# Performance work log

Hardware: AMD Instinct MI355X
Metric: run time of the kernel (lower is better)

Reference implementation:

```python
import jax, jax.numpy as jnp
import numpy as np

N, D_IN, D_HID, D_CODE, K = 131072, 768, 512, 256, 512

def setup_inputs() -> dict:
    key = jax.random.key(0)
    ks = jax.random.split(key, 10)
    s1 = 1.0 / np.sqrt(D_IN); s2 = 1.0 / np.sqrt(D_HID); s3 = 1.0 / np.sqrt(D_CODE)
    return {
        "x": jax.random.normal(ks[0], (N, D_IN), jnp.float32),
        "W1": jax.random.normal(ks[1], (D_IN, D_HID), jnp.float32) * s1,
        "b1": jnp.zeros((D_HID,), jnp.float32),
        "W2": jax.random.normal(ks[2], (D_HID, D_CODE), jnp.float32) * s2,
        "b2": jnp.zeros((D_CODE,), jnp.float32),
        "codebook": jax.random.normal(ks[3], (K, D_CODE), jnp.float32),
        "W3": jax.random.normal(ks[4], (D_CODE, D_HID), jnp.float32) * s3,
        "b3": jnp.zeros((D_HID,), jnp.float32),
        "W4": jax.random.normal(ks[5], (D_HID, D_IN), jnp.float32) * s2,
        "b4": jnp.zeros((D_IN,), jnp.float32),
    }

def reference(x, W1, b1, W2, b2, codebook, W3, b3, W4, b4):
    # encoder: Linear -> ReLU -> Linear
    z = jax.nn.relu(x @ W1 + b1) @ W2 + b2                      # [N, D_CODE]
    # nearest-code search: squared euclidean distances to codebook
    # ||z||^2 - 2 z.c + ||c||^2  (||z||^2 constant per row, drop for argmin)
    dots = z @ codebook.T                                        # [N, K]
    dist = jnp.sum(codebook * codebook, axis=-1)[None, :] - 2.0 * dots
    indices = jnp.argmin(dist, axis=-1)                          # [N] int
    quantized = codebook[indices]                                # gather [N, D_CODE]
    # commitment loss: mse(quantize.detach(), z) * commitment_weight(=1.0)
    commit_loss = jnp.mean((jax.lax.stop_gradient(quantized) - z) ** 2)
    # straight-through estimator
    quantized_st = z + jax.lax.stop_gradient(quantized - z)
    # decoder: Linear -> ReLU -> Linear
    recon = jax.nn.relu(quantized_st @ W3 + b3) @ W4 + b4        # [N, D_IN]
    return recon, indices.astype(jnp.int32), commit_loss
```

## Files before the change

### kernel.cpp

```cpp
#include <hip/hip_runtime.h>
#include <hip/hip_bf16.h>
#include <math.h>

#define N_ROWS 131072
#define DIN    768
#define DHID   512
#define DCODE  256
#define KC     512
#define NFUSE  768
#define TAU    5e-3f

typedef short short8 __attribute__((ext_vector_type(8)));
typedef float f32x4  __attribute__((ext_vector_type(4)));
typedef unsigned int   u32;
typedef unsigned short u16;

__device__ __forceinline__ void gload16(const void* g, void* l) {
    __builtin_amdgcn_global_load_lds(
        (const __attribute__((address_space(1))) u32*)g,
        (__attribute__((address_space(3))) u32*)l, 16, 0, 0);
}

__device__ __forceinline__ u16 f2bf(float f) {
    u32 u = __builtin_bit_cast(u32, f);
    return (u16)((u + 0x7fffu + ((u >> 16) & 1u)) >> 16);
}
__device__ __forceinline__ float bf2f(u16 h) {
    u32 u = ((u32)h) << 16;
    return __builtin_bit_cast(float, u);
}

__device__ __forceinline__ void xcd_swizzle(int& bxs, int& bys) {
    const int GX  = gridDim.x;
    const int nwg = GX * gridDim.y;
    const int lid = blockIdx.y * GX + blockIdx.x;
    const int chunk = nwg >> 3;
    const int nlid  = (lid & 7) * chunk + (lid >> 3);
    bxs = nlid % GX;
    bys = nlid / GX;
}

__device__ __forceinline__ void split_write(char* hidst, char* lodst, float4 v) {
    u16 h0 = f2bf(v.x), h1 = f2bf(v.y), h2 = f2bf(v.z), h3 = f2bf(v.w);
    u16 l0 = f2bf(__fsub_rn(v.x, bf2f(h0)));
    u16 l1 = f2bf(__fsub_rn(v.y, bf2f(h1)));
    u16 l2 = f2bf(__fsub_rn(v.z, bf2f(h2)));
    u16 l3 = f2bf(__fsub_rn(v.w, bf2f(h3)));
    ushort4 hi; hi.x = h0; hi.y = h1; hi.z = h2; hi.w = h3;
    ushort4 lo; lo.x = l0; lo.y = l1; lo.z = l2; lo.w = l3;
    *(ushort4*)hidst = hi;
    *(ushort4*)lodst = lo;
}

template<int EPI>
__global__ __launch_bounds__(256, 3)
void split2_gemm(const float* __restrict__ Af32,
                 const u16* __restrict__ Ahi, const u16* __restrict__ Alo,
                 const u16* __restrict__ Bhi, const u16* __restrict__ Blo,
                 const float* __restrict__ bias,
                 const float* __restrict__ cnorm,
                 u16* __restrict__ Chi, u16* __restrict__ Clo,
                 float* __restrict__ pd1, int* __restrict__ pi1,
                 float* __restrict__ pd2, float* __restrict__ pzn,
                 int M, int N, int K)
{
    __shared__ char lds[32768];
    const int t = threadIdx.x, lane = t & 63, wid = t >> 6;
    const int wm = wid >> 1, wn = wid & 1;
    int bxs, bys; xcd_swizzle(bxs, bys);
    const int bm = bys * 128, bn = bxs * 128;
    const bool full3 = (EPI == 0) || (bxs < 4);

    const int sr = lane >> 3, qq = lane & 7, sl = qq ^ sr;
    const u16* bsrc[4];
    #pragma unroll
    for (int c = 0; c < 4; c++) {
        int row = bn + (wid * 4 + c) * 8 + sr;
        const u16* base = (sl < 4) ? Bhi : Blo;
        bsrc[c] = base + (size_t)row * K + (sl & 3) * 8;
    }
    const u16* asrc[4];
    const float* a32src[4];
    int adhi[4], adlo[4];
    if constexpr (EPI == 1) {
        #pragma unroll
        for (int c = 0; c < 4; c++) {
            int row = bm + (wid * 4 + c) * 8 + sr;
            const u16* base = (sl < 4) ? Ahi : Alo;
            asrc[c] = base + (size_t)row * K + (sl & 3) * 8;
        }
    } else {
        #pragma unroll
        for (int c = 0; c < 4; c++) {
            int id = c * 256 + t;
            int row = id >> 3, k4 = id & 7;
            a32src[c] = Af32 + (size_t)(bm + row) * K + k4 * 4;
            int s = k4 >> 1, hf = k4 & 1;
            adhi[c] = row * 128 + ((s ^ (row & 7)) << 4) + hf * 8;
            adlo[c] = row * 128 + (((s | 4) ^ (row & 7)) << 4) + hf * 8;
        }
    }

    f32x4 acc[4][4];
    #pragma unroll
    for (int i = 0; i < 4; i++)
        #pragma unroll
        for (int j = 0; j < 4; j++) acc[i][j] = (f32x4)0.f;

    const int fr = lane & 15, sw = lane & 7;
    const int offhi = (((lane >> 4) ^ sw) << 4);
    const int offlo = ((((lane >> 4) | 4) ^ sw) << 4);
    const int arow = wm * 64 + fr, brow = wn * 64 + fr;
    const int NT = K >> 5;

    for (int tt = 0; tt < NT; tt++) {
        __syncthreads();
        const int kadv = tt * 32;
        #pragma unroll
        for (int c = 0; c < 4; c++)
            gload16(bsrc[c] + kadv, lds + 16384 + (wid * 4 + c) * 1024);
        if constexpr (EPI == 1) {
            #pragma unroll
            for (int c = 0; c < 4; c++)
                gload16(asrc[c] + kadv, lds + (wid * 4 + c) * 1024);
        } else {
            #pragma unroll
            for (int c = 0; c < 4; c++) {
                float4 v = *(const float4*)(a32src[c] + kadv);
                split_write(lds + adhi[c], lds + adlo[c], v);
            }
        }
        __syncthreads();
        char* ab  = lds;
        char* bb2 = lds + 16384;
        short8 ah[4], al[4];
        #pragma unroll
        for (int i = 0; i < 4; i++) {
            ah[i] = *(const short8*)(ab + ((arow + i * 16) << 7) + offhi);
            al[i] = *(const short8*)(ab + ((arow + i * 16) << 7) + offlo);
        }
        if (full3) {
            #pragma unroll
            for (int j = 0; j < 4; j++) {
                short8 bh = *(const short8*)(bb2 + ((brow + j * 16) << 7) + offhi);
                short8 bl = *(const short8*)(bb2 + ((brow + j * 16) << 7) + offlo);
                #pragma unroll
                for (int i = 0; i < 4; i++) {
                    acc[i][j] = __builtin_amdgcn_mfma_f32_16x16x32_bf16(ah[i], bh, acc[i][j], 0, 0, 0);
                    acc[i][j] = __builtin_amdgcn_mfma_f32_16x16x32_bf16(al[i], bh, acc[i][j], 0, 0, 0);
                    acc[i][j] = __builtin_amdgcn_mfma_f32_16x16x32_bf16(ah[i], bl, acc[i][j], 0, 0, 0);
                }
            }
        } else {
            #pragma unroll
            for (int j = 0; j < 4; j++) {
                short8 bh = *(const short8*)(bb2 + ((brow + j * 16) << 7) + offhi);
                #pragma unroll
                for (int i = 0; i < 4; i++)
                    acc[i][j] = __builtin_amdgcn_mfma_f32_16x16x32_bf16(ah[i], bh, acc[i][j], 0, 0, 0);
            }
        }
    }

    if constexpr (EPI == 1) {
        const int ec = lane & 15, g = lane >> 4;
        if (bxs < 4) {
            float cnv[4], bcv[4];
            #pragma unroll
            for (int j = 0; j < 4; j++) {
                int c = bn + wn * 64 + j * 16 + ec;
                cnv[j] = cnorm[c]; bcv[j] = bias[c];
            }
            const int strip = bxs * 2 + wn;
            #pragma unroll
            for (int i = 0; i < 4; i++) {
                #pragma unroll
                for (int e = 0; e < 4; e++) {
                    float d1 = INFINITY, d2 = INFINITY; int i1 = 0x7fffffff;
                    #pragma unroll
                    for (int j = 0; j < 4; j++) {
                        int c = bn + wn * 64 + j * 16 + ec;
                        float d = __fsub_rn(cnv[j],
                                  __fmul_rn(2.0f, __fadd_rn(acc[i][j][e], bcv[j])));
                        if (d < d1 || (d == d1 && c < i1)) { d2 = d1; d1 = d; i1 = c; }
                        else if (d < d2) d2 = d;
                    }
                    #pragma unroll
                    for (int m = 1; m < 16; m <<= 1) {
                        float od1 = __shfl_xor(d1, m);
                        int   oi1 = __shfl_xor(i1, m);
                        float od2 = __shfl_xor(d2, m);
                        if (od1 < d1 || (od1 == d1 && oi1 < i1)) {
                            d2 = fminf(d1, od2); d1 = od1; i1 = oi1;
                        } else d2 = fminf(d2, od1);
                    }
                    if (ec == 0) {
                        int r = bm + wm * 64 + i * 16 + g * 4 + e;
                        pd1[(size_t)strip * M + r] = d1;
                        pi1[(size_t)strip * M + r] = i1;
                        pd2[(size_t)strip * M + r] = d2;
                    }
                }
            }
        } else {
            float bcv[4];
            #pragma unroll
            for (int j = 0; j < 4; j++)
                bcv[j] = bias[bn + wn * 64 + j * 16 + ec];
            const int zs = (bxs - 4) * 2 + wn;
            #pragma unroll
            for (int i = 0; i < 4; i++) {
                #pragma unroll
                for (int e = 0; e < 4; e++) {
                    float s = 0.f;
                    #pragma unroll
                    for (int j = 0; j < 4; j++) {
                        float zv = acc[i][j][e] + bcv[j];
                        s = fmaf(zv, zv, s);
                    }
                    #pragma unroll
                    for (int m = 1; m < 16; m <<= 1) s += __shfl_xor(s, m);
                    if (ec == 0) {
                        int r = bm + wm * 64 + i * 16 + g * 4 + e;
                        pzn[(size_t)zs * M + r] = s;
                    }
                }
            }
        }
        return;
    } else {
        const int er = (lane >> 4) * 4, ec = lane & 15;
        #pragma unroll
        for (int j = 0; j < 4; j++) {
            int col = bn + wn * 64 + j * 16 + ec;
            float bb = bias[col];
            #pragma unroll
            for (int i = 0; i < 4; i++) {
                #pragma unroll
                for (int e = 0; e < 4; e++) {
                    int r = bm + wm * 64 + i * 16 + er + e;
                    float v = fmaxf(__fadd_rn(acc[i][j][e], bb), 0.f);
                    u16 hi = f2bf(v);
                    u16 lo = f2bf(__fsub_rn(v, bf2f(hi)));
                    Chi[(size_t)r * N + col] = hi;
                    Clo[(size_t)r * N + col] = lo;
                }
            }
        }
    }
}

template<bool RELU, bool OUT_BF16>
__global__ __launch_bounds__(256, 3)
void mfma_gemm(const u16* __restrict__ A, const u16* __restrict__ BT,
               const float* __restrict__ bias,
               void* __restrict__ Cout, int M, int N, int K)
{
    __shared__ char lds[32768];
    const int t    = threadIdx.x;
    const int lane = t & 63, wid = t >> 6;
    const int wm   = wid >> 1, wn = wid & 1;
    int bxs, bys;
    xcd_swizzle(bxs, bys);
    const int bm = bys * 128, bn = bxs * 128;

    const int sr = lane >> 3;
    const int sc = ((lane & 7) ^ sr) * 8;
    const u16* aptr[4];
    const u16* bptr[4];
    #pragma unroll
    for (int c = 0; c < 4; c++) {
        int gc   = wid * 4 + c;
        int arow = bm + 8 * gc + sr;
        aptr[c] = A  + (size_t)arow * K + sc;
        int brow = bn + 8 * gc + sr;
        bptr[c] = BT + (size_t)brow * K + sc;
    }

    f32x4 acc[4][4];
    #pragma unroll
    for (int i = 0; i < 4; i++)
        #pragma unroll
        for (int j = 0; j < 4; j++) acc[i][j] = (f32x4)0.f;

    const int koff0 = (16 * (lane >> 4))      ^ ((lane & 7) << 4);
    const int koff1 = (64 + 16 * (lane >> 4)) ^ ((lane & 7) << 4);
    const int arow_rd = wm * 64 + (lane & 15);
    const int brow_rd = wn * 64 + (lane & 15);

    const int NT = K >> 6;
    for (int tt = 0; tt < NT; tt++) {
        __syncthreads();
        const int k0 = tt << 6;
        #pragma unroll
        for (int c = 0; c < 4; c++) {
            int gc = wid * 4 + c;
            gload16(aptr[c] + k0, lds + gc * 1024);
            gload16(bptr[c] + k0, lds + 16384 + gc * 1024);
        }
        __syncthreads();
        char* ldsA = lds;
        char* ldsB = lds + 16384;
        #pragma unroll
        for (int kk = 0; kk < 2; kk++) {
            const int ko = kk ? koff1 : koff0;
            short8 af[4], bfr[4];
            #pragma unroll
            for (int i = 0; i < 4; i++)
                af[i]  = *(const short8*)(ldsA + (arow_rd + i * 16) * 128 + ko);
            #pragma unroll
            for (int j = 0; j < 4; j++)
                bfr[j] = *(const short8*)(ldsB + (brow_rd + j * 16) * 128 + ko);
            #pragma unroll
            for (int i = 0; i < 4; i++)
                #pragma unroll
                for (int j = 0; j < 4; j++)
                    acc[i][j] = __builtin_amdgcn_mfma_f32_16x16x32_bf16(
                        af[i], bfr[j], acc[i][j], 0, 0, 0);
        }
    }

    const int er = (lane >> 4) * 4;
    const int ec = lane & 15;
    #pragma unroll
    for (int j = 0; j < 4; j++) {
        int col  = bn + wn * 64 + j * 16 + ec;
        float bb = bias[col];
        #pragma unroll
        for (int i = 0; i < 4; i++) {
            #pragma unroll
            for (int e = 0; e < 4; e++) {
                int r   = bm + wm * 64 + i * 16 + er + e;
                float v = acc[i][j][e] + bb;
                if (RELU) v = fmaxf(v, 0.f);
                if (OUT_BF16) ((u16*)Cout)[(size_t)r * N + col]  = f2bf(v);
                else          ((float*)Cout)[(size_t)r * N + col] = v;
            }
        }
    }
}

__global__ __launch_bounds__(256)
void gather_out(const float* __restrict__ R, const int* __restrict__ idxi,
                float* __restrict__ out)
{
    int w    = (blockIdx.x * 256 + threadIdx.x) >> 6;
    int lane = threadIdx.x & 63;
    int nw   = (gridDim.x * 256) >> 6;
    for (int r = w; r < N_ROWS; r += nw) {
        int code = idxi[r];
        const float4* src = (const float4*)(R + (size_t)code * DIN);
        float4* dst = (float4*)(out + (size_t)r * DIN);
        dst[lane]       = src[lane];
        dst[lane + 64]  = src[lane + 64];
        dst[lane + 128] = src[lane + 128];
    }
}

__global__ void transpose_cb_kernel(const float* __restrict__ cb, float* __restrict__ cbT)
{
    int tid = blockIdx.x * 256 + threadIdx.x;
    int k = tid >> 8;
    int d = tid & 255;
    cbT[(size_t)d * KC + k] = cb[(size_t)k * DCODE + d];
}

__global__ void cast_bf16_kernel(const float* __restrict__ in, u16* __restrict__ out, int n)
{
    int i = blockIdx.x * 256 + threadIdx.x;
    if (i < n) out[i] = f2bf(in[i]);
}

__global__ void castT_bf16_kernel(const float* __restrict__ in, u16* __restrict__ out,
                                  int K, int N)
{
    int i = blockIdx.x * 256 + threadIdx.x;
    if (i >= K * N) return;
    int n = i / K, k = i - n * K;
    out[i] = f2bf(in[(size_t)k * N + n]);
}

__global__ void prep_W1T(const float* __restrict__ W1, u16* __restrict__ Thi,
                         u16* __restrict__ Tlo)
{
    int id = blockIdx.x * 256 + threadIdx.x;
    if (id >= DHID * DIN) return;
    int n = id / DIN, k = id - n * DIN;
    float v = W1[(size_t)k * DHID + n];
    u16 hi = f2bf(v);
    Thi[id] = hi;
    Tlo[id] = f2bf(__fsub_rn(v, bf2f(hi)));
}

__global__ void prep_Wc(const float* __restrict__ W2, const float* __restrict__ cb,
                        u16* __restrict__ Thi, u16* __restrict__ Tlo)
{
    int id = blockIdx.x * 256 + threadIdx.x;
    int n = id & 511, h = id >> 9;
    double acc = 0.0;
    for (int tt2 = 0; tt2 < DCODE; tt2++)
        acc += (double)W2[(size_t)h * DCODE + tt2] * (double)cb[(size_t)n * DCODE + tt2];
    float v = (float)acc;
    u16 hi = f2bf(v);
    Thi[(size_t)n * DHID + h] = hi;
    Tlo[(size_t)n * DHID + h] = f2bf(__fsub_rn(v, bf2f(hi)));
}

__global__ void prep_W2T_pair(const float* __restrict__ W2, u16* __restrict__ Thi,
                              u16* __restrict__ Tlo)
{
    int id = blockIdx.x * 256 + threadIdx.x;
    if (id >= DCODE * DHID) return;
    int t2 = id >> 9, h = id & 511;
    float v = W2[(size_t)h * DCODE + t2];
    u16 hi = f2bf(v);
    Thi[(size_t)(KC + t2) * DHID + h] = hi;
    Tlo[(size_t)(KC + t2) * DHID + h] = f2bf(__fsub_rn(v, bf2f(hi)));
}

__global__ void prep_bcf(const float* __restrict__ b2, const float* __restrict__ cb,
                         float* __restrict__ bcf)
{
    int n = blockIdx.x * 256 + threadIdx.x;
    if (n >= NFUSE) return;
    if (n < KC) {
        double acc = 0.0;
        for (int tt2 = 0; tt2 < DCODE; tt2++)
            acc += (double)b2[tt2] * (double)cb[(size_t)n * DCODE + tt2];
        bcf[n] = (float)acc;
    } else {
        bcf[n] = b2[n - KC];
    }
}

__global__ void cnorm_np_kernel(const float* __restrict__ cb, float* __restrict__ cnorm)
{
    int k = blockIdx.x * 64 + threadIdx.x;
    if (k >= KC) return;
    const float* c = cb + (size_t)k * DCODE;
    float bsum[2];
    #pragma unroll
    for (int b = 0; b < 2; b++) {
        const float* a = c + b * 128;
        float r[8];
        #pragma unroll
        for (int j = 0; j < 8; j++) r[j] = __fmul_rn(a[j], a[j]);
        for (int i = 8; i < 128; i += 8)
            #pragma unroll
            for (int j = 0; j < 8; j++)
                r[j] = __fadd_rn(r[j], __fmul_rn(a[i + j], a[i + j]));
        bsum[b] = __fadd_rn(
            __fadd_rn(__fadd_rn(r[0], r[1]), __fadd_rn(r[2], r[3])),
            __fadd_rn(__fadd_rn(r[4], r[5]), __fadd_rn(r[6], r[7])));
    }
    cnorm[k] = __fadd_rn(bsum[0], bsum[1]);
}

__global__ void final_argmin_flag(const float* __restrict__ pd1,
                                  const int* __restrict__ pi1,
                                  const float* __restrict__ pd2,
                                  const float* __restrict__ pzn,
                                  float* __restrict__ idx_f,
                                  int* __restrict__ idx_i,
                                  float* __restrict__ rowloss,
                                  int* __restrict__ cnt,
                                  int* __restrict__ list)
{
    int r = blockIdx.x * 256 + threadIdx.x;
    if (r >= N_ROWS) return;
    float d1 = pd1[r]; int i1 = pi1[r]; float d2 = pd2[r];
    #pragma unroll
    for (int b = 1; b < 8; b++) {
        float od1 = pd1[(size_t)b * N_ROWS + r];
        int   oi1 = pi1[(size_t)b * N_ROWS + r];
        float od2 = pd2[(size_t)b * N_ROWS + r];
        if (od1 < d1 || (od1 == d1 && oi1 < i1)) {
            d2 = fminf(d1, od2); d1 = od1; i1 = oi1;
        } else d2 = fminf(d2, od1);
    }
    float zn = pzn[r] + pzn[(size_t)N_ROWS + r]
             + pzn[(size_t)2 * N_ROWS + r] + pzn[(size_t)3 * N_ROWS + r];
    idx_f[r]   = (float)i1;
    idx_i[r]   = i1;
    rowloss[r] = zn + d1;
    if (d2 - d1 < TAU) {
        int p = atomicAdd(cnt, 1);
        list[p] = r;
    }
}

__global__ __launch_bounds__(512)
void recompute_kernel(const float* __restrict__ x,  const float* __restrict__ W1,
                      const float* __restrict__ b1, const float* __restrict__ W2,
                      const float* __restrict__ b2, const float* __restrict__ cbT,
                      const float* __restrict__ cnorm,
                      const int* __restrict__ cnt,  const int* __restrict__ list,
                      float* __restrict__ idx_f,    int* __restrict__ idx_i)
{
    __shared__ float xs[8][DIN];
    __shared__ float h1s[8][DHID];
    __shared__ float zs[8][DCODE];
    __shared__ float swd[8][8];
    __shared__ int   swi[8][8];
    __shared__ int   rls[8];
    const int t = threadIdx.x;
    const int n = *cnt;

    for (int base = blockIdx.x * 8; base < n; base += gridDim.x * 8) {
        __syncthreads();
        if (t < 8) rls[t] = (base + t < n) ? list[base + t] : -1;
        __syncthreads();
        #pragma unroll
        for (int rr = 0; rr < 8; rr++) {
            int row = rls[rr];
            if (row >= 0)
                for (int i = t; i < DIN; i += 512)
                    xs[rr][i] = x[(size_t)row * DIN + i];
        }
        __syncthreads();
        {
            float acc[8] = {0.f,0.f,0.f,0.f,0.f,0.f,0.f,0.f};
            for (int i = 0; i < DIN; i++) {
                float w = W1[(size_t)i * DHID + t];
                #pragma unroll
                for (int rr = 0; rr < 8; rr++)
                    acc[rr] = fmaf(xs[rr][i], w, acc[rr]);
            }
            float bb = b1[t];
            #pragma unroll
            for (int rr = 0; rr < 8; rr++)
                h1s[rr][t] = fmaxf(__fadd_rn(acc[rr], bb), 0.f);
        }
        __syncthreads();
        {
            int half = t >> 8, t2 = t & 255;
            float acc[4] = {0.f,0.f,0.f,0.f};
            for (int h = 0; h < DHID; h++) {
                float w = W2[(size_t)h * DCODE + t2];
                #pragma unroll
                for (int q2 = 0; q2 < 4; q2++)
                    acc[q2] = fmaf(h1s[half * 4 + q2][h], w, acc[q2]);
            }
            float bb = b2[t2];
            #pragma unroll
            for (int q2 = 0; q2 < 4; q2++)
                zs[half * 4 + q2][t2] = __fadd_rn(acc[q2], bb);
        }
        __syncthreads();
        {
            float acc[8] = {0.f,0.f,0.f,0.f,0.f,0.f,0.f,0.f};
            for (int d = 0; d < DCODE; d++) {
                float c = cbT[(size_t)d * KC + t];
                #pragma unroll
                for (int rr = 0; rr < 8; rr++)
                    acc[rr] = fmaf(zs[rr][d], c, acc[rr]);
            }
            float cn = cnorm[t];
            #pragma unroll
            for (int rr = 0; rr < 8; rr++) {
                float d = __fsub_rn(cn, __fmul_rn(2.0f, acc[rr]));
                int ii = t;
                #pragma unroll
                for (int m = 1; m < 64; m <<= 1) {
                    float od = __shfl_xor(d, m);
                    int   oi = __shfl_xor(ii, m);
                    if (od < d || (od == d && oi < ii)) { d = od; ii = oi; }
                }
                if ((t & 63) == 0) { swd[rr][t >> 6] = d; swi[rr][t >> 6] = ii; }
            }
        }
        __syncthreads();
        if (t < 8) {
            int row = rls[t];
            if (row >= 0) {
                float d = swd[t][0]; int ii = swi[t][0];
                #pragma unroll
                for (int w = 1; w < 8; w++) {
                    float od = swd[t][w]; int oi = swi[t][w];
                    if (od < d || (od == d && oi < ii)) { d = od; ii = oi; }
                }
                idx_i[row] = ii;
                idx_f[row] = (float)ii;
            }
        }
    }
}

__global__ void loss_reduce_kernel(const float* __restrict__ rowloss,
                                   double* __restrict__ acc, int n)
{
    double s = 0.0;
    for (int i = blockIdx.x * blockDim.x + threadIdx.x; i < n; i += gridDim.x * blockDim.x)
        s += (double)rowloss[i];
    for (int off = 32; off; off >>= 1) s += __shfl_xor(s, off);
    __shared__ double red[4];
    int lane = threadIdx.x & 63, wave = threadIdx.x >> 6;
    if (lane == 0) red[wave] = s;
    __syncthreads();
    if (threadIdx.x == 0) {
        double b = red[0] + red[1] + red[2] + red[3];
        atomicAdd(acc, b);
    }
}

__global__ void finalize_kernel(const double* __restrict__ acc, float* __restrict__ out)
{
    out[0] = (float)(acc[0] / ((double)N_ROWS * (double)DCODE));
}

extern "C" void kernel_launch(void* const* d_in, const int* in_sizes, int n_in,
                              void* d_out, int out_size, void* d_ws, size_t ws_size,
                              hipStream_t stream)
{
    const float* x  = (const float*)d_in[0];
    const float* W1 = (const float*)d_in[1];
    const float* b1 = (const float*)d_in[2];
    const float* W2 = (const float*)d_in[3];
    const float* b2 = (const float*)d_in[4];
    const float* cb = (const float*)d_in[5];
    const float* W3 = (const float*)d_in[6];
    const float* b3 = (const float*)d_in[7];
    const float* W4 = (const float*)d_in[8];
    const float* b4 = (const float*)d_in[9];
    float* out = (float*)d_out;
    char*  ws  = (char*)d_ws;

    u16*    h1hi    = (u16*)   (ws);
    u16*    h1lo    = (u16*)   (ws + 134217728);
    float*  pd1     = (float*) (ws + 268435456);
    int*    pi1     = (int*)   (ws + 272629760);
    float*  pd2     = (float*) (ws + 276824064);
    float*  pzn     = (float*) (ws + 281018368);
    float*  rowloss = (float*) (ws + 283115520);
    int*    idxi    = (int*)   (ws + 283639808);
    int*    list    = (int*)   (ws + 284164096);
    int*    rcnt    = (int*)   (ws + 284688384);
    double* lossa   = (double*)(ws + 284688448);
    u16*    W1Thi   = (u16*)   (ws + 284688512);
    u16*    W1Tlo   = (u16*)   (ws + 285474944);
    u16*    WfThi   = (u16*)   (ws + 286261376);
    u16*    WfTlo   = (u16*)   (ws + 287047808);
    u16*    cbB     = (u16*)   (ws + 287834240);
    u16*    W3T     = (u16*)   (ws + 288096384);
    u16*    W4T     = (u16*)   (ws + 288358528);
    float*  bcf     = (float*) (ws + 289144960);
    float*  cnorm   = (float*) (ws + 289148032);
    float*  cbT     = (float*) (ws + 289150080);
    u16*    R1b     = (u16*)   (ws + 289674368);
    float*  Rf      = (float*) (ws + 290198656);

    float* idxf    = out + (size_t)N_ROWS * DIN;
    float* lossout = idxf + N_ROWS;

    hipMemsetAsync(ws + 284688384, 0, 128, stream);

    transpose_cb_kernel<<<512, 256, 0, stream>>>(cb, cbT);
    cnorm_np_kernel<<<8, 64, 0, stream>>>(cb, cnorm);
    cast_bf16_kernel<<<(KC*DCODE)/256, 256, 0, stream>>>(cb, cbB, KC*DCODE);
    castT_bf16_kernel<<<(DCODE*DHID)/256, 256, 0, stream>>>(W3, W3T, DCODE, DHID);
    castT_bf16_kernel<<<(DHID*DIN)/256, 256, 0, stream>>>(W4, W4T, DHID, DIN);
    prep_W1T<<<(DHID*DIN)/256, 256, 0, stream>>>(W1, W1Thi, W1Tlo);
    prep_Wc<<<(KC*DHID)/256, 256, 0, stream>>>(W2, cb, WfThi, WfTlo);
    prep_W2T_pair<<<(DCODE*DHID)/256, 256, 0, stream>>>(W2, WfThi, WfTlo);
    prep_bcf<<<3, 256, 0, stream>>>(b2, cb, bcf);

    mfma_gemm<true,  true ><<<dim3(4, 4), 256, 0, stream>>>(
        cbB, W3T, b3, (void*)R1b, KC, DHID, DCODE);
    mfma_gemm<false, false><<<dim3(6, 4), 256, 0, stream>>>(
        R1b, W4T, b4, (void*)Rf, KC, DIN, DHID);

    split2_gemm<0><<<dim3(DHID/128, N_ROWS/128), 256, 0, stream>>>(
        x, nullptr, nullptr, W1Thi, W1Tlo, b1, nullptr,
        h1hi, h1lo, nullptr, nullptr, nullptr, nullptr, N_ROWS, DHID, DIN);
    split2_gemm<1><<<dim3(NFUSE/128, N_ROWS/128), 256, 0, stream>>>(
        nullptr, h1hi, h1lo, WfThi, WfTlo, bcf, cnorm,
        nullptr, nullptr, pd1, pi1, pd2, pzn, N_ROWS, NFUSE, DHID);

    final_argmin_flag<<<N_ROWS/256, 256, 0, stream>>>(
        pd1, pi1, pd2, pzn, idxf, idxi, rowloss, rcnt, list);
    recompute_kernel<<<2048, 512, 0, stream>>>(
        x, W1, b1, W2, b2, cbT, cnorm, rcnt, list, idxf, idxi);

    gather_out<<<4096, 256, 0, stream>>>(Rf, idxi, out);

    loss_reduce_kernel<<<256, 256, 0, stream>>>(rowloss, lossa, N_ROWS);
    finalize_kernel<<<1, 1, 0, stream>>>(lossa, lossout);
}
```

Before: 942.0 us.

## Use single-bf16 dots GEMM with split-precision rescoring of ambiguous rows

```diff
diff --git a/kernel.cpp b/kernel.cpp
--- a/kernel.cpp
+++ b/kernel.cpp
@@ -8,7 +8,9 @@
 #define DCODE  256
 #define KC     512
 #define NFUSE  768
-#define TAU    5e-3f
+#define TAU1   0.6f
+#define TAU2   5e-3f
+#define CAP    16384
 
 typedef short short8 __attribute__((ext_vector_type(8)));
 typedef float f32x4  __attribute__((ext_vector_type(4)));
@@ -61,7 +63,7 @@
                  const float* __restrict__ cnorm,
                  u16* __restrict__ Chi, u16* __restrict__ Clo,
                  float* __restrict__ pd1, int* __restrict__ pi1,
-                 float* __restrict__ pd2, float* __restrict__ pzn,
+                 float* __restrict__ pd2,
                  int M, int N, int K)
 {
     __shared__ char lds[32768];
@@ -69,7 +71,6 @@
     const int wm = wid >> 1, wn = wid & 1;
     int bxs, bys; xcd_swizzle(bxs, bys);
     const int bm = bys * 128, bn = bxs * 128;
-    const bool full3 = (EPI == 0) || (bxs < 4);
 
     const int sr = lane >> 3, qq = lane & 7, sl = qq ^ sr;
     const u16* bsrc[4];
@@ -139,91 +140,55 @@
             ah[i] = *(const short8*)(ab + ((arow + i * 16) << 7) + offhi);
             al[i] = *(const short8*)(ab + ((arow + i * 16) << 7) + offlo);
         }
-        if (full3) {
-            #pragma unroll
-            for (int j = 0; j < 4; j++) {
-                short8 bh = *(const short8*)(bb2 + ((brow + j * 16) << 7) + offhi);
-                short8 bl = *(const short8*)(bb2 + ((brow + j * 16) << 7) + offlo);
-                #pragma unroll
-                for (int i = 0; i < 4; i++) {
-                    acc[i][j] = __builtin_amdgcn_mfma_f32_16x16x32_bf16(ah[i], bh, acc[i][j], 0, 0, 0);
-                    acc[i][j] = __builtin_amdgcn_mfma_f32_16x16x32_bf16(al[i], bh, acc[i][j], 0, 0, 0);
-                    acc[i][j] = __builtin_amdgcn_mfma_f32_16x16x32_bf16(ah[i], bl, acc[i][j], 0, 0, 0);
-                }
-            }
-        } else {
-            #pragma unroll
-            for (int j = 0; j < 4; j++) {
-                short8 bh = *(const short8*)(bb2 + ((brow + j * 16) << 7) + offhi);
-                #pragma unroll
-                for (int i = 0; i < 4; i++)
-                    acc[i][j] = __builtin_amdgcn_mfma_f32_16x16x32_bf16(ah[i], bh, acc[i][j], 0, 0, 0);
+        #pragma unroll
+        for (int j = 0; j < 4; j++) {
+            short8 bh = *(const short8*)(bb2 + ((brow + j * 16) << 7) + offhi);
+            short8 bl = *(const short8*)(bb2 + ((brow + j * 16) << 7) + offlo);
+            #pragma unroll
+            for (int i = 0; i < 4; i++) {
+                acc[i][j] = __builtin_amdgcn_mfma_f32_16x16x32_bf16(ah[i], bh, acc[i][j], 0, 0, 0);
+                acc[i][j] = __builtin_amdgcn_mfma_f32_16x16x32_bf16(al[i], bh, acc[i][j], 0, 0, 0);
+                acc[i][j] = __builtin_amdgcn_mfma_f32_16x16x32_bf16(ah[i], bl, acc[i][j], 0, 0, 0);
             }
         }
     }
 
     if constexpr (EPI == 1) {
         const int ec = lane & 15, g = lane >> 4;
-        if (bxs < 4) {
-            float cnv[4], bcv[4];
-            #pragma unroll
-            for (int j = 0; j < 4; j++) {
-                int c = bn + wn * 64 + j * 16 + ec;
-                cnv[j] = cnorm[c]; bcv[j] = bias[c];
-            }
-            const int strip = bxs * 2 + wn;
-            #pragma unroll
-            for (int i = 0; i < 4; i++) {
-                #pragma unroll
-                for (int e = 0; e < 4; e++) {
-                    float d1 = INFINITY, d2 = INFINITY; int i1 = 0x7fffffff;
-                    #pragma unroll
-                    for (int j = 0; j < 4; j++) {
-                        int c = bn + wn * 64 + j * 16 + ec;
-                        float d = __fsub_rn(cnv[j],
-                                  __fmul_rn(2.0f, __fadd_rn(acc[i][j][e], bcv[j])));
-                        if (d < d1 || (d == d1 && c < i1)) { d2 = d1; d1 = d; i1 = c; }
-                        else if (d < d2) d2 = d;
-                    }
-                    #pragma unroll
-                    for (int m = 1; m < 16; m <<= 1) {
-                        float od1 = __shfl_xor(d1, m);
-                        int   oi1 = __shfl_xor(i1, m);
-                        float od2 = __shfl_xor(d2, m);
-                        if (od1 < d1 || (od1 == d1 && oi1 < i1)) {
-                            d2 = fminf(d1, od2); d1 = od1; i1 = oi1;
-                        } else d2 = fminf(d2, od1);
-                    }
-                    if (ec == 0) {
-                        int r = bm + wm * 64 + i * 16 + g * 4 + e;
-                        pd1[(size_t)strip * M + r] = d1;
-                        pi1[(size_t)strip * M + r] = i1;
-                        pd2[(size_t)strip * M + r] = d2;
-                    }
-                }
-            }
-        } else {
-            float bcv[4];
-            #pragma unroll
-            for (int j = 0; j < 4; j++)
-                bcv[j] = bias[bn + wn * 64 + j * 16 + ec];
-            const int zs = (bxs - 4) * 2 + wn;
-            #pragma unroll
-            for (int i = 0; i < 4; i++) {
-                #pragma unroll
-                for (int e = 0; e < 4; e++) {
-                    float s = 0.f;
-                    #pragma unroll
-                    for (int j = 0; j < 4; j++) {
-                        float zv = acc[i][j][e] + bcv[j];
-                        s = fmaf(zv, zv, s);
-                    }
-                    #pragma unroll
-                    for (int m = 1; m < 16; m <<= 1) s += __shfl_xor(s, m);
-                    if (ec == 0) {
-                        int r = bm + wm * 64 + i * 16 + g * 4 + e;
-                        pzn[(size_t)zs * M + r] = s;
-                    }
+        float cnv[4], bcv[4];
+        #pragma unroll
+        for (int j = 0; j < 4; j++) {
+            int c = bn + wn * 64 + j * 16 + ec;
+            cnv[j] = cnorm[c]; bcv[j] = bias[c];
+        }
+        const int strip = bxs * 2 + wn;
+        #pragma unroll
+        for (int i = 0; i < 4; i++) {
+            #pragma unroll
+            for (int e = 0; e < 4; e++) {
+                float d1 = INFINITY, d2 = INFINITY; int i1 = 0x7fffffff;
+                #pragma unroll
+                for (int j = 0; j < 4; j++) {
+                    int c = bn + wn * 64 + j * 16 + ec;
+                    float d = __fsub_rn(cnv[j],
+                              __fmul_rn(2.0f, __fadd_rn(acc[i][j][e], bcv[j])));
+                    if (d < d1 || (d == d1 && c < i1)) { d2 = d1; d1 = d; i1 = c; }
+                    else if (d < d2) d2 = d;
+                }
+                #pragma unroll
+                for (int m = 1; m < 16; m <<= 1) {
+                    float od1 = __shfl_xor(d1, m);
+                    int   oi1 = __shfl_xor(i1, m);
+                    float od2 = __shfl_xor(d2, m);
+                    if (od1 < d1 || (od1 == d1 && oi1 < i1)) {
+                        d2 = fminf(d1, od2); d1 = od1; i1 = oi1;
+                    } else d2 = fminf(d2, od1);
+                }
+                if (ec == 0) {
+                    int r = bm + wm * 64 + i * 16 + g * 4 + e;
+                    pd1[(size_t)strip * M + r] = d1;
+                    pi1[(size_t)strip * M + r] = i1;
+                    pd2[(size_t)strip * M + r] = d2;
                 }
             }
         }
@@ -250,6 +215,139 @@
     }
 }
 
+__global__ __launch_bounds__(256, 3)
+void dots_gemm(const u16* __restrict__ A, const u16* __restrict__ BT,
+               const float* __restrict__ bias, const float* __restrict__ cnorm,
+               float* __restrict__ pd1, int* __restrict__ pi1,
+               float* __restrict__ pd2, float* __restrict__ pzn,
+               int M, int N, int K)
+{
+    __shared__ char lds[32768];
+    const int t = threadIdx.x, lane = t & 63, wid = t >> 6;
+    const int wm = wid >> 1, wn = wid & 1;
+    int bxs, bys; xcd_swizzle(bxs, bys);
+    const int bm = bys * 128, bn = bxs * 128;
+
+    const int sr = lane >> 3;
+    const int sc = ((lane & 7) ^ sr) * 8;
+    const u16* aptr[4];
+    const u16* bptr[4];
+    #pragma unroll
+    for (int c = 0; c < 4; c++) {
+        int gc = wid * 4 + c;
+        aptr[c] = A  + (size_t)(bm + 8 * gc + sr) * K + sc;
+        bptr[c] = BT + (size_t)(bn + 8 * gc + sr) * K + sc;
+    }
+
+    f32x4 acc[4][4];
+    #pragma unroll
+    for (int i = 0; i < 4; i++)
+        #pragma unroll
+        for (int j = 0; j < 4; j++) acc[i][j] = (f32x4)0.f;
+
+    const int koff0 = (16 * (lane >> 4))      ^ ((lane & 7) << 4);
+    const int koff1 = (64 + 16 * (lane >> 4)) ^ ((lane & 7) << 4);
+    const int arow_rd = wm * 64 + (lane & 15);
+    const int brow_rd = wn * 64 + (lane & 15);
+
+    const int NT = K >> 6;
+    for (int tt = 0; tt < NT; tt++) {
+        __syncthreads();
+        const int k0 = tt << 6;
+        #pragma unroll
+        for (int c = 0; c < 4; c++) {
+            int gc = wid * 4 + c;
+            gload16(aptr[c] + k0, lds + gc * 1024);
+            gload16(bptr[c] + k0, lds + 16384 + gc * 1024);
+        }
+        __syncthreads();
+        char* ldsA = lds;
+        char* ldsB = lds + 16384;
+        #pragma unroll
+        for (int kk = 0; kk < 2; kk++) {
+            const int ko = kk ? koff1 : koff0;
+            short8 af[4], bfr[4];
+            #pragma unroll
+            for (int i = 0; i < 4; i++)
+                af[i]  = *(const short8*)(ldsA + (arow_rd + i * 16) * 128 + ko);
+            #pragma unroll
+            for (int j = 0; j < 4; j++)
+                bfr[j] = *(const short8*)(ldsB + (brow_rd + j * 16) * 128 + ko);
+            #pragma unroll
+            for (int i = 0; i < 4; i++)
+                #pragma unroll
+                for (int j = 0; j < 4; j++)
+                    acc[i][j] = __builtin_amdgcn_mfma_f32_16x16x32_bf16(
+                        af[i], bfr[j], acc[i][j], 0, 0, 0);
+        }
+    }
+
+    const int ec = lane & 15, g = lane >> 4;
+    if (bxs < 4) {
+        float cnv[4], bcv[4];
+        #pragma unroll
+        for (int j = 0; j < 4; j++) {
+            int c = bn + wn * 64 + j * 16 + ec;
+            cnv[j] = cnorm[c]; bcv[j] = bias[c];
+        }
+        const int strip = bxs * 2 + wn;
+        #pragma unroll
+        for (int i = 0; i < 4; i++) {
+            #pragma unroll
+            for (int e = 0; e < 4; e++) {
+                float d1 = INFINITY, d2 = INFINITY; int i1 = 0x7fffffff;
+                #pragma unroll
+                for (int j = 0; j < 4; j++) {
+                    int c = bn + wn * 64 + j * 16 + ec;
+                    float d = __fsub_rn(cnv[j],
+                              __fmul_rn(2.0f, __fadd_rn(acc[i][j][e], bcv[j])));
+                    if (d < d1 || (d == d1 && c < i1)) { d2 = d1; d1 = d; i1 = c; }
+                    else if (d < d2) d2 = d;
+                }
+                #pragma unroll
+                for (int m = 1; m < 16; m <<= 1) {
+                    float od1 = __shfl_xor(d1, m);
+                    int   oi1 = __shfl_xor(i1, m);
+                    float od2 = __shfl_xor(d2, m);
+                    if (od1 < d1 || (od1 == d1 && oi1 < i1)) {
+                        d2 = fminf(d1, od2); d1 = od1; i1 = oi1;
+                    } else d2 = fminf(d2, od1);
+                }
+                if (ec == 0) {
+                    int r = bm + wm * 64 + i * 16 + g * 4 + e;
+                    pd1[(size_t)strip * M + r] = d1;
+                    pi1[(size_t)strip * M + r] = i1;
+                    pd2[(size_t)strip * M + r] = d2;
+                }
+            }
+        }
+    } else {
+        float bcv[4];
+        #pragma unroll
+        for (int j = 0; j < 4; j++)
+            bcv[j] = bias[bn + wn * 64 + j * 16 + ec];
+        const int zs = (bxs - 4) * 2 + wn;
+        #pragma unroll
+        for (int i = 0; i < 4; i++) {
+            #pragma unroll
+            for (int e = 0; e < 4; e++) {
+                float s = 0.f;
+                #pragma unroll
+                for (int j = 0; j < 4; j++) {
+                    float zv = acc[i][j][e] + bcv[j];
+                    s = fmaf(zv, zv, s);
+                }
+                #pragma unroll
+                for (int m = 1; m < 16; m <<= 1) s += __shfl_xor(s, m);
+                if (ec == 0) {
+                    int r = bm + wm * 64 + i * 16 + g * 4 + e;
+                    pzn[(size_t)zs * M + r] = s;
+                }
+            }
+        }
+    }
+}
+
 template<bool RELU, bool OUT_BF16>
 __global__ __launch_bounds__(256, 3)
 void mfma_gemm(const u16* __restrict__ A, const u16* __restrict__ BT,
@@ -271,10 +369,8 @@
     #pragma unroll
     for (int c = 0; c < 4; c++) {
         int gc   = wid * 4 + c;
-        int arow = bm + 8 * gc + sr;
-        aptr[c] = A  + (size_t)arow * K + sc;
-        int brow = bn + 8 * gc + sr;
-        bptr[c] = BT + (size_t)brow * K + sc;
+        aptr[c] = A  + (size_t)(bm + 8 * gc + sr) * K + sc;
+        bptr[c] = BT + (size_t)(bn + 8 * gc + sr) * K + sc;
     }
 
     f32x4 acc[4][4];
@@ -406,16 +502,12 @@
     Tlo[(size_t)n * DHID + h] = f2bf(__fsub_rn(v, bf2f(hi)));
 }
 
-__global__ void prep_W2T_pair(const float* __restrict__ W2, u16* __restrict__ Thi,
-                              u16* __restrict__ Tlo)
+__global__ void prep_W2T(const float* __restrict__ W2, u16* __restrict__ T)
 {
     int id = blockIdx.x * 256 + threadIdx.x;
     if (id >= DCODE * DHID) return;
     int t2 = id >> 9, h = id & 511;
-    float v = W2[(size_t)h * DCODE + t2];
-    u16 hi = f2bf(v);
-    Thi[(size_t)(KC + t2) * DHID + h] = hi;
-    Tlo[(size_t)(KC + t2) * DHID + h] = f2bf(__fsub_rn(v, bf2f(hi)));
+    T[(size_t)(KC + t2) * DHID + h] = f2bf(W2[(size_t)h * DCODE + t2]);
 }
 
 __global__ void prep_bcf(const float* __restrict__ b2, const float* __restrict__ cb,
@@ -483,9 +575,68 @@
     idx_f[r]   = (float)i1;
     idx_i[r]   = i1;
     rowloss[r] = zn + d1;
-    if (d2 - d1 < TAU) {
+    if (d2 - d1 < TAU1) {
         int p = atomicAdd(cnt, 1);
         list[p] = r;
+    }
+}
+
+__global__ void gather_h1(const u16* __restrict__ h1hi, const u16* __restrict__ h1lo,
+                          const int* __restrict__ list, const int* __restrict__ cnt,
+                          u16* __restrict__ ghi, u16* __restrict__ glo)
+{
+    int n1 = *cnt; if (n1 > CAP) n1 = CAP;
+    int total = n1 * 64;
+    for (int c = blockIdx.x * blockDim.x + threadIdx.x; c < total;
+         c += gridDim.x * blockDim.x) {
+        int i = c >> 6, o = (c & 63) * 8;
+        int row = list[i];
+        *(short8*)(ghi + (size_t)i * DHID + o) =
+            *(const short8*)(h1hi + (size_t)row * DHID + o);
+        *(short8*)(glo + (size_t)i * DHID + o) =
+            *(const short8*)(h1lo + (size_t)row * DHID + o);
+    }
+}
+
+__global__ void merge2_flag(const float* __restrict__ pd1b,
+                            const int* __restrict__ pi1b,
+                            const float* __restrict__ pd2b,
+                            const int* __restrict__ list,
+                            const int* __restrict__ cnt1,
+                            float* __restrict__ idx_f, int* __restrict__ idx_i,
+                            int* __restrict__ cnt2, int* __restrict__ list2)
+{
+    int i = blockIdx.x * 256 + threadIdx.x;
+    if (i >= CAP) return;
+    int n1 = *cnt1; if (n1 > CAP) n1 = CAP;
+    if (i >= n1) return;
+    float d1 = pd1b[i]; int i1 = pi1b[i]; float d2 = pd2b[i];
+    #pragma unroll
+    for (int b = 1; b < 8; b++) {
+        float od1 = pd1b[(size_t)b * CAP + i];
+        int   oi1 = pi1b[(size_t)b * CAP + i];
+        float od2 = pd2b[(size_t)b * CAP + i];
+        if (od1 < d1 || (od1 == d1 && oi1 < i1)) {
+            d2 = fminf(d1, od2); d1 = od1; i1 = oi1;
+        } else d2 = fminf(d2, od1);
+    }
+    int row = list[i];
+    idx_f[row] = (float)i1;
+    idx_i[row] = i1;
+    if (d2 - d1 < TAU2) {
+        int p = atomicAdd(cnt2, 1);
+        list2[p] = row;
+    }
+}
+
+__global__ void overflow_append(const int* __restrict__ list,
+                                const int* __restrict__ cnt1,
+                                int* __restrict__ cnt2, int* __restrict__ list2)
+{
+    int i = CAP + blockIdx.x * 256 + threadIdx.x;
+    if (i < *cnt1) {
+        int p = atomicAdd(cnt2, 1);
+        list2[p] = list[i];
     }
 }
 
@@ -631,28 +782,35 @@
     int*    pi1     = (int*)   (ws + 272629760);
     float*  pd2     = (float*) (ws + 276824064);
     float*  pzn     = (float*) (ws + 281018368);
-    float*  rowloss = (float*) (ws + 283115520);
-    int*    idxi    = (int*)   (ws + 283639808);
-    int*    list    = (int*)   (ws + 284164096);
-    int*    rcnt    = (int*)   (ws + 284688384);
-    double* lossa   = (double*)(ws + 284688448);
-    u16*    W1Thi   = (u16*)   (ws + 284688512);
-    u16*    W1Tlo   = (u16*)   (ws + 285474944);
-    u16*    WfThi   = (u16*)   (ws + 286261376);
-    u16*    WfTlo   = (u16*)   (ws + 287047808);
-    u16*    cbB     = (u16*)   (ws + 287834240);
-    u16*    W3T     = (u16*)   (ws + 288096384);
-    u16*    W4T     = (u16*)   (ws + 288358528);
-    float*  bcf     = (float*) (ws + 289144960);
-    float*  cnorm   = (float*) (ws + 289148032);
-    float*  cbT     = (float*) (ws + 289150080);
-    u16*    R1b     = (u16*)   (ws + 289674368);
-    float*  Rf      = (float*) (ws + 290198656);
+    float*  pd1b    = (float*) (ws + 283115520);
+    int*    pi1b    = (int*)   (ws + 283639808);
+    float*  pd2b    = (float*) (ws + 284164096);
+    u16*    h1ghi   = (u16*)   (ws + 284688384);
+    u16*    h1glo   = (u16*)   (ws + 301465600);
+    float*  rowloss = (float*) (ws + 318242816);
+    int*    idxi    = (int*)   (ws + 318767104);
+    int*    list    = (int*)   (ws + 319291392);
+    int*    list2   = (int*)   (ws + 319815680);
+    int*    rcnt1   = (int*)   (ws + 320339968);
+    int*    rcnt2   = (int*)   (ws + 320339972);
+    double* lossa   = (double*)(ws + 320340032);
+    u16*    W1Thi   = (u16*)   (ws + 320340096);
+    u16*    W1Tlo   = (u16*)   (ws + 321126528);
+    u16*    Wfb     = (u16*)   (ws + 321912960);
+    u16*    WfTlo   = (u16*)   (ws + 322699392);
+    u16*    cbB     = (u16*)   (ws + 323223680);
+    u16*    W3T     = (u16*)   (ws + 323485824);
+    u16*    W4T     = (u16*)   (ws + 323747968);
+    float*  bcf     = (float*) (ws + 324534400);
+    float*  cnorm   = (float*) (ws + 324537472);
+    float*  cbT     = (float*) (ws + 324539520);
+    u16*    R1b     = (u16*)   (ws + 325063808);
+    float*  Rf      = (float*) (ws + 325588096);
 
     float* idxf    = out + (size_t)N_ROWS * DIN;
     float* lossout = idxf + N_ROWS;
 
-    hipMemsetAsync(ws + 284688384, 0, 128, stream);
+    hipMemsetAsync(ws + 320339968, 0, 128, stream);
 
     transpose_cb_kernel<<<512, 256, 0, stream>>>(cb, cbT);
     cnorm_np_kernel<<<8, 64, 0, stream>>>(cb, cnorm);
@@ -660,8 +818,8 @@
     castT_bf16_kernel<<<(DCODE*DHID)/256, 256, 0, stream>>>(W3, W3T, DCODE, DHID);
     castT_bf16_kernel<<<(DHID*DIN)/256, 256, 0, stream>>>(W4, W4T, DHID, DIN);
     prep_W1T<<<(DHID*DIN)/256, 256, 0, stream>>>(W1, W1Thi, W1Tlo);
-    prep_Wc<<<(KC*DHID)/256, 256, 0, stream>>>(W2, cb, WfThi, WfTlo);
-    prep_W2T_pair<<<(DCODE*DHID)/256, 256, 0, stream>>>(W2, WfThi, WfTlo);
+    prep_Wc<<<(KC*DHID)/256, 256, 0, stream>>>(W2, cb, Wfb, WfTlo);
+    prep_W2T<<<(DCODE*DHID)/256, 256, 0, stream>>>(W2, Wfb);
     prep_bcf<<<3, 256, 0, stream>>>(b2, cb, bcf);
 
     mfma_gemm<true,  true ><<<dim3(4, 4), 256, 0, stream>>>(
@@ -671,15 +829,22 @@
 
     split2_gemm<0><<<dim3(DHID/128, N_ROWS/128), 256, 0, stream>>>(
         x, nullptr, nullptr, W1Thi, W1Tlo, b1, nullptr,
-        h1hi, h1lo, nullptr, nullptr, nullptr, nullptr, N_ROWS, DHID, DIN);
-    split2_gemm<1><<<dim3(NFUSE/128, N_ROWS/128), 256, 0, stream>>>(
-        nullptr, h1hi, h1lo, WfThi, WfTlo, bcf, cnorm,
-        nullptr, nullptr, pd1, pi1, pd2, pzn, N_ROWS, NFUSE, DHID);
-
+        h1hi, h1lo, nullptr, nullptr, nullptr, N_ROWS, DHID, DIN);
+    dots_gemm<<<dim3(NFUSE/128, N_ROWS/128), 256, 0, stream>>>(
+        h1hi, Wfb, bcf, cnorm, pd1, pi1, pd2, pzn, N_ROWS, NFUSE, DHID);
     final_argmin_flag<<<N_ROWS/256, 256, 0, stream>>>(
-        pd1, pi1, pd2, pzn, idxf, idxi, rowloss, rcnt, list);
+        pd1, pi1, pd2, pzn, idxf, idxi, rowloss, rcnt1, list);
+
+    gather_h1<<<512, 256, 0, stream>>>(h1hi, h1lo, list, rcnt1, h1ghi, h1glo);
+    split2_gemm<1><<<dim3(KC/128, CAP/128), 256, 0, stream>>>(
+        nullptr, h1ghi, h1glo, Wfb, WfTlo, bcf, cnorm,
+        nullptr, nullptr, pd1b, pi1b, pd2b, CAP, KC, DHID);
+    merge2_flag<<<CAP/256, 256, 0, stream>>>(
+        pd1b, pi1b, pd2b, list, rcnt1, idxf, idxi, rcnt2, list2);
+    overflow_append<<<(N_ROWS-CAP)/256, 256, 0, stream>>>(list, rcnt1, rcnt2, list2);
+
     recompute_kernel<<<2048, 512, 0, stream>>>(
-        x, W1, b1, W2, b2, cbT, cnorm, rcnt, list, idxf, idxi);
+        x, W1, b1, W2, b2, cbT, cnorm, rcnt2, list2, idxf, idxi);
 
     gather_out<<<4096, 256, 0, stream>>>(Rf, idxi, out);
 
```

Result: faster. 879.5 us (-6.6%).
